# Optimization experiments

Hardware: AMD Instinct MI355X
Metric: run time of the kernel (lower is better)

## Reference

```python
import jax, jax.numpy as jnp
import numpy as np
import math

B, L, D, NUM_TYPES = 4, 4096, 512, 22
T_MAX = 200.0
SIGMA, LAMBD = 10.0, 0.005


def setup_inputs() -> dict:
    key = jax.random.key(0)
    k1, k2, k3 = jax.random.split(key, 3)
    event_type = jax.random.randint(k1, (B, L), 0, NUM_TYPES + 1)
    # event times in [0, t_max), sorted along the sequence (realistic point process)
    event_time = jnp.sort(jax.random.uniform(k2, (B, L), dtype=jnp.float32) * T_MAX, axis=-1)
    # embedding table with padding row 0 zeroed (padding_idx=0)
    emb_table = jax.random.normal(k3, (NUM_TYPES + 1, D), dtype=jnp.float32).at[0].set(0.0)
    return {"event_type": event_type, "event_time": event_time, "emb_table": emb_table}


def reference(event_type, event_time, emb_table):
    d_model = emb_table.shape[1]
    seq_len = event_time.shape[1]

    # sinusoidal temporal encoding: t / 10000^(2*(i//2)/d)
    i = jnp.arange(d_model)
    pos_vec = jnp.power(jnp.float32(10000.0), 2.0 * (i // 2).astype(jnp.float32) / d_model)
    temp = event_time[:, :, None] / pos_vec  # [B, L, D]
    temp_enc = jnp.where(i % 2 == 0, jnp.sin(temp), jnp.cos(temp))

    type_embedding = emb_table[event_type] * math.sqrt(d_model)  # [B, L, D]
    embedding = jnp.concatenate([temp_enc, type_embedding], axis=-1)  # [B, L, 2D]

    # RBF kernel pairwise scores: sigma^2 * exp(-(|ti - tj|^norm)^2 / lambd^2), norm=2
    t = event_time / T_MAX  # normalized times
    d = jnp.abs(t[:, :, None] - t[:, None, :]) ** 2  # [B, L, L]
    scores = (SIGMA ** 2) * jnp.exp(-(d ** 2) / (LAMBD ** 2))

    # causal mask: keep j <= i, fill future with -1000, then softmax over rows
    causal = jnp.tril(jnp.ones((seq_len, seq_len), dtype=bool))  # [L, L]
    scores = jnp.where(causal[None, :, :], scores, jnp.float32(-1000.0))
    scores = jax.nn.softmax(scores, axis=-1)
    return scores, embedding
```

## Files before the change

kernel.cpp:

```cpp
#include <hip/hip_runtime.h>

#define SEQ_L 4096
#define BATCH 4
#define DMODEL 512
#define CUT 0.055f
#define RPW 8
#define RPB 32
#define SCORE_BLOCKS (BATCH * SEQ_L / RPB)
#define EMB_BLOCKS 512
#define EMB_RPB (BATCH * SEQ_L / EMB_BLOCKS)

typedef float f4 __attribute__((ext_vector_type(4)));

__device__ __forceinline__ void nt_store4(f4* p, f4 v) {
    __builtin_nontemporal_store(v, p);
}

__global__ __launch_bounds__(256) void fused_kernel(const int* __restrict__ et,
                                                    const float* __restrict__ tm,
                                                    const float* __restrict__ tab,
                                                    float* __restrict__ scores,
                                                    float* __restrict__ emb) {
    if (blockIdx.x < SCORE_BLOCKS) {
        __shared__ float ts[SEQ_L];
        const int b  = blockIdx.x / (SEQ_L / RPB);
        const int i0 = (blockIdx.x % (SEQ_L / RPB)) * RPB;

        const f4* tb4 = (const f4*)(tm + b * SEQ_L);
        f4* ts4 = (f4*)ts;
        #pragma unroll
        for (int q = 0; q < 4; ++q) {
            int j = threadIdx.x + q * 256;
            ts4[j] = tb4[j] * (1.0f / 200.0f);
        }
        __syncthreads();

        const int wave = threadIdx.x >> 6;
        const int lane = threadIdx.x & 63;
        const int ibase = i0 + wave * RPW;

        float tiR[RPW], invR[RPW];
        int   jloR[RPW];

        int jlo;
        {
            const float tc = ts[ibase] - CUT;
            int lo = 0, hi = ibase;
            while (lo < hi) {
                int mid = (lo + hi) >> 1;
                if (ts[mid] < tc) lo = mid + 1; else hi = mid;
            }
            jlo = lo;
        }

        #pragma unroll
        for (int r = 0; r < RPW; ++r) {
            const int i = ibase + r;
            const float ti = ts[i];
            const float tc = ti - CUT;
            for (;;) {
                int idx = jlo + lane; if (idx > SEQ_L - 1) idx = SEQ_L - 1;
                int cnt = __popcll(__ballot(ts[idx] < tc));
                jlo += cnt;
                if (cnt < 64) break;
            }
            float sum = 0.0f;
            for (int j = jlo + lane; j <= i; j += 64) {
                float d = ti - ts[j];
                float d2 = d * d;
                float s = 100.0f * __expf(-(d2 * d2) * 40000.0f);
                sum += __expf(s - 100.0f);
            }
            #pragma unroll
            for (int off = 1; off < 64; off <<= 1) sum += __shfl_xor(sum, off, 64);
            tiR[r] = ti; invR[r] = 1.0f / sum; jloR[r] = jlo;
        }

        #pragma unroll
        for (int r = 0; r < RPW; ++r) {
            const int i = ibase + r;
            const float ti = tiR[r], inv = invR[r];
            const int jl = jloR[r];
            const int c_lo = jl >> 2, c_hi = i >> 2;
            f4* out4 = (f4*)(scores + ((size_t)(b * SEQ_L + i)) * SEQ_L);
            const f4 z = {0.0f, 0.0f, 0.0f, 0.0f};

            for (int c = lane; c < c_lo; c += 64)
                nt_store4(out4 + c, z);
            for (int c = c_lo + lane; c <= c_hi; c += 64) {
                f4 tv = ts4[c];
                f4 v;
                #pragma unroll
                for (int q = 0; q < 4; ++q) {
                    const int jj = 4 * c + q;
                    float d = ti - tv[q];
                    float d2 = d * d;
                    float s = 100.0f * __expf(-(d2 * d2) * 40000.0f);
                    float p = __expf(s - 100.0f) * inv;
                    v[q] = (jj >= jl && jj <= i) ? p : 0.0f;
                }
                nt_store4(out4 + c, v);
            }
            for (int c = c_hi + 1 + lane; c < SEQ_L / 4; c += 64)
                nt_store4(out4 + c, z);
        }
    } else {
        const int t = threadIdx.x;
        const bool temporal = t < 128;

        float ipA = 0.0f, ipB = 0.0f;
        if (temporal) {
            const float c = -13.287712379549449f / 256.0f;
            ipA = exp2f(c * (float)(2 * t));
            ipB = exp2f(c * (float)(2 * t + 1));
        }
        const int ecol = (t - 128) * 4;

        const int bl0 = ((int)blockIdx.x - SCORE_BLOCKS) * EMB_RPB;
        for (int r = 0; r < EMB_RPB; ++r) {
            const int bl = bl0 + r;
            f4 v;
            if (temporal) {
                const float time = tm[bl];
                const float a = time * ipA;
                const float bp = time * ipB;
                v[0] = __sinf(a);  v[1] = __cosf(a);
                v[2] = __sinf(bp); v[3] = __cosf(bp);
            } else {
                f4 e = *(const f4*)(tab + et[bl] * DMODEL + ecol);
                v = e * 22.627416997969522f;
            }
            nt_store4((f4*)(emb + (size_t)bl * 2 * DMODEL) + t, v);
        }
    }
}

extern "C" void kernel_launch(void* const* d_in, const int* in_sizes, int n_in,
                              void* d_out, int out_size, void* d_ws, size_t ws_size,
                              hipStream_t stream) {
    const int*   event_type = (const int*)d_in[0];
    const float* event_time = (const float*)d_in[1];
    const float* emb_table  = (const float*)d_in[2];

    float* scores = (float*)d_out;
    float* emb    = scores + (size_t)BATCH * SEQ_L * SEQ_L;

    fused_kernel<<<SCORE_BLOCKS + EMB_BLOCKS, 256, 0, stream>>>(
        event_type, event_time, emb_table, scores, emb);
}
```

Baseline: 78.11 us.

## Issue zero-fill stores before softmax sums, use plain stores, halve rows per block

Reorders the score path so the zero-fill stores for the masked and far-past regions of each row go out before the exp/sum reduction, letting the write traffic overlap the compute. Nontemporal stores are replaced with ordinary stores in both the score and embedding paths. Rows per wave and per block are halved, which doubles the score block count and shortens each block's work. The tradeoffs are more ts shared-memory staging per row processed, and ordinary stores may pollute cache on a write-bound kernel.

New measurement: 67.30 us. 13.8% less time.

```diff
diff --git a/kernel.cpp b/kernel.cpp
--- a/kernel.cpp
+++ b/kernel.cpp
@@ -4,17 +4,13 @@
 #define BATCH 4
 #define DMODEL 512
 #define CUT 0.055f
-#define RPW 8
-#define RPB 32
+#define RPW 4
+#define RPB 16
 #define SCORE_BLOCKS (BATCH * SEQ_L / RPB)
 #define EMB_BLOCKS 512
 #define EMB_RPB (BATCH * SEQ_L / EMB_BLOCKS)
 
 typedef float f4 __attribute__((ext_vector_type(4)));
-
-__device__ __forceinline__ void nt_store4(f4* p, f4 v) {
-    __builtin_nontemporal_store(v, p);
-}
 
 __global__ __launch_bounds__(256) void fused_kernel(const int* __restrict__ et,
                                                     const float* __restrict__ tm,
@@ -39,9 +35,8 @@
         const int lane = threadIdx.x & 63;
         const int ibase = i0 + wave * RPW;
 
-        float tiR[RPW], invR[RPW];
         int   jloR[RPW];
-
+        float tiR[RPW];
         int jlo;
         {
             const float tc = ts[ibase] - CUT;
@@ -52,11 +47,9 @@
             }
             jlo = lo;
         }
-
         #pragma unroll
         for (int r = 0; r < RPW; ++r) {
-            const int i = ibase + r;
-            const float ti = ts[i];
+            const float ti = ts[ibase + r];
             const float tc = ti - CUT;
             for (;;) {
                 int idx = jlo + lane; if (idx > SEQ_L - 1) idx = SEQ_L - 1;
@@ -64,8 +57,26 @@
                 jlo += cnt;
                 if (cnt < 64) break;
             }
+            jloR[r] = jlo; tiR[r] = ti;
+        }
+
+        const f4 z = {0.0f, 0.0f, 0.0f, 0.0f};
+        #pragma unroll
+        for (int r = 0; r < RPW; ++r) {
+            const int i = ibase + r;
+            const int c_lo = jloR[r] >> 2, c_hi = i >> 2;
+            f4* out4 = (f4*)(scores + ((size_t)(b * SEQ_L + i)) * SEQ_L);
+            for (int c = lane; c < c_lo; c += 64)                  out4[c] = z;
+            for (int c = c_hi + 1 + lane; c < SEQ_L / 4; c += 64)  out4[c] = z;
+        }
+
+        float invR[RPW];
+        #pragma unroll
+        for (int r = 0; r < RPW; ++r) {
+            const int i = ibase + r;
+            const float ti = tiR[r];
             float sum = 0.0f;
-            for (int j = jlo + lane; j <= i; j += 64) {
+            for (int j = jloR[r] + lane; j <= i; j += 64) {
                 float d = ti - ts[j];
                 float d2 = d * d;
                 float s = 100.0f * __expf(-(d2 * d2) * 40000.0f);
@@ -73,7 +84,7 @@
             }
             #pragma unroll
             for (int off = 1; off < 64; off <<= 1) sum += __shfl_xor(sum, off, 64);
-            tiR[r] = ti; invR[r] = 1.0f / sum; jloR[r] = jlo;
+            invR[r] = 1.0f / sum;
         }
 
         #pragma unroll
@@ -83,10 +94,6 @@
             const int jl = jloR[r];
             const int c_lo = jl >> 2, c_hi = i >> 2;
             f4* out4 = (f4*)(scores + ((size_t)(b * SEQ_L + i)) * SEQ_L);
-            const f4 z = {0.0f, 0.0f, 0.0f, 0.0f};
-
-            for (int c = lane; c < c_lo; c += 64)
-                nt_store4(out4 + c, z);
             for (int c = c_lo + lane; c <= c_hi; c += 64) {
                 f4 tv = ts4[c];
                 f4 v;
@@ -99,10 +106,8 @@
                     float p = __expf(s - 100.0f) * inv;
                     v[q] = (jj >= jl && jj <= i) ? p : 0.0f;
                 }
-                nt_store4(out4 + c, v);
+                out4[c] = v;
             }
-            for (int c = c_hi + 1 + lane; c < SEQ_L / 4; c += 64)
-                nt_store4(out4 + c, z);
         }
     } else {
         const int t = threadIdx.x;
@@ -130,7 +135,7 @@
                 f4 e = *(const f4*)(tab + et[bl] * DMODEL + ecol);
                 v = e * 22.627416997969522f;
             }
-            nt_store4((f4*)(emb + (size_t)bl * 2 * DMODEL) + t, v);
+            ((f4*)(emb + (size_t)bl * 2 * DMODEL))[t] = v;
         }
     }
 }
```
